# Performance work log

Measured on AMD Instinct MI355X. Metric: run time of the kernel, lower is better.

## Reference

```python
import jax, jax.numpy as jnp
import numpy as np
import math

N = 10000      # nodes (batched protein residues)
E = 160000     # edges (avg degree 16)
D = 1280       # node/hidden dim (ESM2-650M)
M = 24         # message_dim
EE = 16        # edge_embedding_dim (sinusoidal distance features)
L = 6          # num EGNN layers
LN_EPS = 1e-5


def setup_inputs() -> dict:
    key = jax.random.key(0)
    ks = jax.random.split(key, 20)
    s = 0.02
    h = jax.random.normal(ks[0], (N, D), jnp.float32)
    pos = jax.random.normal(ks[1], (N, 3), jnp.float32) * 10.0
    edge_index = jax.random.randint(ks[2], (2, E), 0, N, jnp.int32)
    msg_in_dim = 2 * D + EE + 1  # h_i, h_j, edge_attr, radial
    params = dict(
        node_emb_W=jax.random.normal(ks[3], (D, D), jnp.float32) * s,
        node_emb_b=jnp.zeros((D,), jnp.float32),
        msg_W1=jax.random.normal(ks[4], (L, msg_in_dim, M), jnp.float32) * s,
        msg_b1=jnp.zeros((L, M), jnp.float32),
        msg_W2=jax.random.normal(ks[5], (L, M, M), jnp.float32) * s,
        msg_b2=jnp.zeros((L, M), jnp.float32),
        coord_W1=jax.random.normal(ks[6], (L - 1, M, M), jnp.float32) * s,
        coord_b1=jnp.zeros((L - 1, M), jnp.float32),
        coord_W2=jax.random.normal(ks[7], (L - 1, M, 1), jnp.float32) * s,  # no bias
        node_W1=jax.random.normal(ks[8], (L, D + M, M), jnp.float32) * s,
        node_b1=jnp.zeros((L, M), jnp.float32),
        node_W2=jax.random.normal(ks[9], (L, M, D), jnp.float32) * s,
        node_b2=jnp.zeros((L, D), jnp.float32),
        ln_g=jnp.ones((L, D), jnp.float32),
        ln_b=jnp.zeros((L, D), jnp.float32),
    )
    return dict(h=h, pos=pos, edge_index=edge_index, **params)


def reference(h, pos, edge_index, node_emb_W, node_emb_b, msg_W1, msg_b1,
              msg_W2, msg_b2, coord_W1, coord_b1, coord_W2,
              node_W1, node_b1, node_W2, node_b2, ln_g, ln_b):
    row, col = edge_index[0], edge_index[1]  # PyG: row=source j, col=target i

    # sinusoidal distance embedding from initial coordinates (computed once)
    freqs = jnp.exp(-math.log(10000.0) * jnp.arange(0, EE, 2, dtype=jnp.float32) / EE)
    d0 = pos[row] - pos[col]                      # (E,3)
    dist = jnp.sqrt(jnp.sum(d0 * d0, axis=1))     # (E,)
    ang = dist[:, None] * freqs[None, :]          # (E, EE/2)
    edge_attr = jnp.stack([jnp.sin(ang), jnp.cos(ang)], axis=2).reshape(dist.shape[0], EE)

    h = h @ node_emb_W + node_emb_b

    # mean-aggregation denominator: in-degree of target nodes, clamped to 1
    deg = jax.ops.segment_sum(jnp.ones_like(dist), col, num_segments=N)
    denom = jnp.maximum(deg, 1.0)[:, None]

    for l in range(L):
        cd = pos[row] - pos[col]                  # (E,3) coord_diff
        radial = jnp.sum(cd * cd, axis=1, keepdims=True)
        msg_in = jnp.concatenate([h[col], h[row], edge_attr, radial], axis=-1)  # (E, 2D+EE+1)
        msg = jax.nn.silu(jax.nn.silu(msg_in @ msg_W1[l] + msg_b1[l]) @ msg_W2[l] + msg_b2[l])
        msg_agg = jax.ops.segment_sum(msg, col, num_segments=N) / denom  # scatter-mean
        if l < L - 1:  # update_coords for all but last layer
            w = jax.nn.silu(msg @ coord_W1[l] + coord_b1[l]) @ coord_W2[l]  # (E,1)
            pos = pos + jax.ops.segment_sum(cd * w, col, num_segments=N)   # index_add
        h_up = jax.nn.silu(jnp.concatenate([h, msg_agg], axis=-1) @ node_W1[l] + node_b1[l]) @ node_W2[l] + node_b2[l]
        hn = h + h_up
        mu = jnp.mean(hn, axis=-1, keepdims=True)
        var = jnp.mean((hn - mu) ** 2, axis=-1, keepdims=True)
        h = (hn - mu) / jnp.sqrt(var + LN_EPS) * ln_g[l] + ln_b[l]
        # dropout is identity in eval mode
    return h, pos
```

## Files before the change

### kernel.cpp

```cpp
#include <hip/hip_runtime.h>

#define NN 10000
#define NE 160000
#define DD 1280
#define MM 24

typedef __attribute__((ext_vector_type(8))) short bf16x8;
typedef __attribute__((ext_vector_type(4))) float f32x4;
typedef unsigned short u16;

#define O_nembW 0
#define O_nembB 1638400
#define O_msgW1 1639680
#define O_msgB1 2010880
#define O_msgW2 2011136
#define O_msgB2 2014592
#define O_cW1   2014848
#define O_cB1   2017792
#define O_cW2   2017920
#define O_nW1   2018048
#define O_nB1   2205824
#define O_nW2   2206080
#define O_nB2   2390400
#define O_lnG   2398080
#define O_lnB   2405760
#define TOTW    2413440

__device__ __forceinline__ float b2f(u16 u){
  union { unsigned int i; float f; } v; v.i = ((unsigned int)u) << 16; return v.f;
}
__device__ __forceinline__ u16 f2b(float f){
  union { float f; unsigned int i; } v; v.f = f;
  return (u16)((v.i + 0x7fffu + ((v.i >> 16) & 1u)) >> 16);
}
__device__ __forceinline__ float silu_f(float x){ return x / (1.f + __expf(-x)); }

__device__ __forceinline__ void gll16(const u16* g, u16* l){
  __builtin_amdgcn_global_load_lds(
      (const __attribute__((address_space(1))) void*)g,
      (__attribute__((address_space(3))) void*)l, 16, 0, 0);
}

__global__ __launch_bounds__(256) void k_sniff(const u16* __restrict__ h0, int* __restrict__ modep)
{
  __shared__ int cnt;
  if (threadIdx.x == 0) cnt = 0;
  __syncthreads();
  int local = 0;
  for (int i = threadIdx.x; i < 16384; i += 256){
    unsigned int e = (h0[i] >> 7) & 0xFF;
    if (e >= 0xE0) local++;
  }
  atomicAdd(&cnt, local);
  __syncthreads();
  if (threadIdx.x == 0) *modep = (cnt > 16) ? 0 : 1;
}

__global__ __launch_bounds__(256) void k_cvtw(const int* __restrict__ modep,
    const void* p0, const void* p1, const void* p2, const void* p3, const void* p4,
    const void* p5, const void* p6, const void* p7, const void* p8, const void* p9,
    const void* p10, const void* p11, const void* p12, const void* p13, const void* p14,
    u16* __restrict__ wbf)
{
  int i = blockIdx.x * 256 + threadIdx.x;
  if (i >= TOTW) return;
  int mode = *modep;
  const void* src; int j; int sz;
  if      (i < O_nembB){ src = p0;  j = i - O_nembW; sz = 1638400; }
  else if (i < O_msgW1){ src = p1;  j = i - O_nembB; sz = 1280; }
  else if (i < O_msgB1){ src = p2;  j = i - O_msgW1; sz = 371088; }
  else if (i < O_msgW2){ src = p3;  j = i - O_msgB1; sz = 144; }
  else if (i < O_msgB2){ src = p4;  j = i - O_msgW2; sz = 3456; }
  else if (i < O_cW1)  { src = p5;  j = i - O_msgB2; sz = 144; }
  else if (i < O_cB1)  { src = p6;  j = i - O_cW1;   sz = 2880; }
  else if (i < O_cW2)  { src = p7;  j = i - O_cB1;   sz = 120; }
  else if (i < O_nW1)  { src = p8;  j = i - O_cW2;   sz = 120; }
  else if (i < O_nB1)  { src = p9;  j = i - O_nW1;   sz = 187776; }
  else if (i < O_nW2)  { src = p10; j = i - O_nB1;   sz = 144; }
  else if (i < O_nB2)  { src = p11; j = i - O_nW2;   sz = 184320; }
  else if (i < O_lnG)  { src = p12; j = i - O_nB2;   sz = 7680; }
  else if (i < O_lnB)  { src = p13; j = i - O_lnG;   sz = 7680; }
  else                 { src = p14; j = i - O_lnB;   sz = 7680; }
  u16 v = 0;
  if (j < sz) v = mode ? ((const u16*)src)[j] : f2b(((const float*)src)[j]);
  wbf[i] = v;
}

__global__ __launch_bounds__(256) void k_tr(const u16* __restrict__ win, u16* __restrict__ wout)
{
  __shared__ u16 tile[32][33];
  int bx = blockIdx.x % 40, by = blockIdx.x / 40;
  int tc = threadIdx.x & 31, tr = threadIdx.x >> 5;
  #pragma unroll
  for (int p = 0; p < 4; p++){
    int r = p*8 + tr;
    tile[r][tc] = win[(size_t)(by*32 + r)*1280 + bx*32 + tc];
  }
  __syncthreads();
  #pragma unroll
  for (int p = 0; p < 4; p++){
    int r = p*8 + tr;
    wout[(size_t)(bx*32 + r)*1280 + by*32 + tc] = tile[tc][r];
  }
}

__global__ __launch_bounds__(256) void k_packproj(const u16* __restrict__ wbf, u16* __restrict__ wproj)
{
  int i = blockIdx.x * 256 + threadIdx.x;
  if (i >= 6*80*1280) return;
  int l = i / (80*1280);
  int rem = i - l*80*1280;
  int n = rem / 1280;
  int k = rem - n*1280;
  u16 v = 0;
  if (n < 24)       v = wbf[O_msgW1 + (size_t)l*2577*24 + (size_t)k*24 + n];
  else if (n < 48)  v = wbf[O_msgW1 + (size_t)l*2577*24 + (size_t)(1280+k)*24 + (n-24)];
  else if (n < 72)  v = wbf[O_nW1   + (size_t)l*1304*24 + (size_t)k*24 + (n-48)];
  wproj[i] = v;
}

__global__ __launch_bounds__(256) void k_packw2(const u16* __restrict__ wbf, u16* __restrict__ wn2p)
{
  int i = blockIdx.x * 256 + threadIdx.x;
  int l = i / (1280*32); int rem = i - l*1280*32;
  int n = rem >> 5, k = rem & 31;
  wn2p[i] = (k < 24) ? wbf[O_nW2 + (size_t)l*24*1280 + (size_t)k*1280 + n] : (u16)0;
}

__global__ __launch_bounds__(256) void k_cvth(const void* h0, const int* __restrict__ modep,
                                              u16* __restrict__ h0b)
{
  int i = blockIdx.x * 256 + threadIdx.x;
  if (*modep){
    ((int4*)h0b)[i] = ((const int4*)h0)[i];
  } else {
    const float* s = (const float*)h0 + (size_t)i*8;
    bf16x8 o;
    #pragma unroll
    for (int j = 0; j < 8; j++) o[j] = (short)f2b(s[j]);
    *(bf16x8*)(h0b + (size_t)i*8) = o;
  }
}

__global__ __launch_bounds__(256) void k_setup(const void* pos0, const int* __restrict__ modep,
    float* __restrict__ deg, float* __restrict__ posf, float* __restrict__ posf0)
{
  int i = blockIdx.x * 256 + threadIdx.x;
  int mode = *modep;
  if (i < NN) deg[i] = 0.f;
  if (i < NN * 3){
    float p = mode ? b2f(((const u16*)pos0)[i]) : ((const float*)pos0)[i];
    posf[i] = p; posf0[i] = p;
  }
}

__global__ __launch_bounds__(256) void k_deg(const int* __restrict__ eidx, float* __restrict__ deg)
{
  int e = blockIdx.x * 256 + threadIdx.x;
  atomicAdd(&deg[eidx[NE + e]], 1.f);
}

__global__ __launch_bounds__(256) void k_prefix(const float* __restrict__ deg,
                                                int* __restrict__ offs, int* __restrict__ cursor)
{
  __shared__ int part[256];
  int t = threadIdx.x;
  int lo = t * 40, hi = lo + 40; if (hi > NN) hi = NN; if (lo > NN) lo = NN;
  int s = 0;
  for (int i = lo; i < hi; i++) s += (int)deg[i];
  part[t] = s;
  __syncthreads();
  for (int off = 1; off < 256; off <<= 1){
    int v = (t >= off) ? part[t - off] : 0;
    __syncthreads();
    part[t] += v;
    __syncthreads();
  }
  int run = (t == 0) ? 0 : part[t - 1];
  for (int i = lo; i < hi; i++){
    offs[i] = run;
    run += (int)deg[i];
    cursor[i] = 0;
  }
  if (t == 255) offs[NN] = run;
}

__global__ __launch_bounds__(256) void k_scatter(const int* __restrict__ eidx,
    const int* __restrict__ offs, int* __restrict__ cursor, int* __restrict__ perm)
{
  int e = blockIdx.x * 256 + threadIdx.x;
  int cg = eidx[NE + e];
  int p = atomicAdd(&cursor[cg], 1);
  perm[offs[cg] + p] = e;
}

__global__ __launch_bounds__(256) void k_gemm_init(const u16* __restrict__ h0b,
    const u16* __restrict__ wembT, const u16* __restrict__ wbf, u16* __restrict__ Cb)
{
  __shared__ u16 As[128*32];
  __shared__ u16 Bs[128*32];
  int t = threadIdx.x;
  int lane = t & 63, wv = t >> 6;
  int bm = blockIdx.x % 79, bn = blockIdx.x / 79;
  int m0 = bm * 128, n0 = bn * 128;
  int col = lane & 15, quad = lane >> 4;
  int wm = wv & 1, wn = wv >> 1;
  f32x4 acc[4][4];
  #pragma unroll
  for (int mi = 0; mi < 4; mi++)
    #pragma unroll
    for (int ni = 0; ni < 4; ni++) acc[mi][ni] = (f32x4){0.f,0.f,0.f,0.f};

  for (int k0 = 0; k0 < DD; k0 += 32){
    #pragma unroll
    for (int is = 0; is < 2; is++){
      int flat = is*256 + t;
      int row = flat >> 2, seg = flat & 3;
      int grow = m0 + row; if (grow > NN-1) grow = NN-1;
      gll16(h0b + (size_t)grow*DD + k0 + seg*8, As + flat*8);
    }
    #pragma unroll
    for (int is = 0; is < 2; is++){
      int flat = is*256 + t;
      int row = flat >> 2, seg = flat & 3;
      gll16(wembT + (size_t)(n0 + row)*DD + k0 + seg*8, Bs + flat*8);
    }
    __builtin_amdgcn_s_waitcnt(0x0f70);
    __syncthreads();
    bf16x8 af[4], bfv[4];
    #pragma unroll
    for (int mi = 0; mi < 4; mi++)
      af[mi] = *(const bf16x8*)&As[(wm*64 + mi*16 + col)*32 + quad*8];
    #pragma unroll
    for (int ni = 0; ni < 4; ni++)
      bfv[ni] = *(const bf16x8*)&Bs[(wn*64 + ni*16 + col)*32 + quad*8];
    #pragma unroll
    for (int mi = 0; mi < 4; mi++)
      #pragma unroll
      for (int ni = 0; ni < 4; ni++)
        acc[mi][ni] = __builtin_amdgcn_mfma_f32_16x16x32_bf16(af[mi], bfv[ni], acc[mi][ni], 0, 0, 0);
    __syncthreads();
  }
  #pragma unroll
  for (int ni = 0; ni < 4; ni++){
    int cc = n0 + wn*64 + ni*16 + col;
    float bias = b2f(wbf[O_nembB + cc]);
    #pragma unroll
    for (int mi = 0; mi < 4; mi++){
      #pragma unroll
      for (int rr = 0; rr < 4; rr++){
        int row = m0 + wm*64 + mi*16 + quad*4 + rr;
        if (row < NN) Cb[(size_t)row*DD + cc] = f2b(acc[mi][ni][rr] + bias);
      }
    }
  }
}

__global__ __launch_bounds__(128) void k_gemm_proj(const u16* __restrict__ hbm,
    const u16* __restrict__ wproj, int layer,
    float* __restrict__ Ab, float* __restrict__ Bb, float* __restrict__ Mb)
{
  __shared__ u16 As[32*32];
  __shared__ u16 Bs[80*32];
  int t = threadIdx.x;
  int lane = t & 63, wv = t >> 6;
  int m0 = blockIdx.x * 32;
  int col = lane & 15, quad = lane >> 4;
  const u16* wp = wproj + (size_t)layer * 80 * 1280;
  f32x4 acc[5];
  #pragma unroll
  for (int ni = 0; ni < 5; ni++) acc[ni] = (f32x4){0.f,0.f,0.f,0.f};

  for (int k0 = 0; k0 < DD; k0 += 32){
    { int row = t >> 2, seg = t & 3;
      int grow = m0 + row; if (grow > NN-1) grow = NN-1;
      gll16(hbm + (size_t)grow*DD + k0 + seg*8, As + t*8); }
    #pragma unroll
    for (int is = 0; is < 3; is++){
      int flat = is*128 + t;
      if (flat < 320){
        int row = flat >> 2, seg = flat & 3;
        gll16(wp + (size_t)row*DD + k0 + seg*8, Bs + flat*8);
      }
    }
    __builtin_amdgcn_s_waitcnt(0x0f70);
    __syncthreads();
    bf16x8 af = *(const bf16x8*)&As[(wv*16 + col)*32 + quad*8];
    #pragma unroll
    for (int ni = 0; ni < 5; ni++){
      bf16x8 bv = *(const bf16x8*)&Bs[(ni*16 + col)*32 + quad*8];
      acc[ni] = __builtin_amdgcn_mfma_f32_16x16x32_bf16(af, bv, acc[ni], 0, 0, 0);
    }
    __syncthreads();
  }
  #pragma unroll
  for (int ni = 0; ni < 5; ni++){
    int n = ni*16 + col;
    if (n < 72){
      int rg = (n >= 48) ? 2 : (n >= 24 ? 1 : 0);
      int cc = n - rg*24;
      float* base = (rg == 0) ? Ab : (rg == 1) ? Bb : Mb;
      #pragma unroll
      for (int rr = 0; rr < 4; rr++){
        int m = m0 + wv*16 + quad*4 + rr;
        if (m < NN) base[m*24 + cc] = acc[ni][rr];
      }
    }
  }
}

__global__ __launch_bounds__(256) void k_edge(const int* __restrict__ eidx,
    const float* __restrict__ posf, const float* __restrict__ posf0,
    const float* __restrict__ Ab, const float* __restrict__ Bb,
    const u16* __restrict__ wbf, int layer, int do_coord,
    u16* __restrict__ msgu, float* __restrict__ wcdbuf)
{
  __shared__ float sW1e[16*24], sWr[24], sB1[24], sW2[24*24], sB2[24];
  __shared__ float sCW1[24*24], sCB1[24], sCW2[24];
  int t = threadIdx.x;
  const u16* w1l = wbf + O_msgW1 + (size_t)layer * 2577 * 24;
  for (int i = t; i < 16*24; i += 256) sW1e[i] = b2f(w1l[2560*24 + i]);
  for (int i = t; i < 24; i += 256){
    sWr[i] = b2f(w1l[2576*24 + i]);
    sB1[i] = b2f(wbf[O_msgB1 + layer*24 + i]);
    sB2[i] = b2f(wbf[O_msgB2 + layer*24 + i]);
  }
  for (int i = t; i < 576; i += 256) sW2[i] = b2f(wbf[O_msgW2 + layer*576 + i]);
  if (do_coord){
    for (int i = t; i < 576; i += 256) sCW1[i] = b2f(wbf[O_cW1 + layer*576 + i]);
    for (int i = t; i < 24; i += 256){
      sCB1[i] = b2f(wbf[O_cB1 + layer*24 + i]);
      sCW2[i] = b2f(wbf[O_cW2 + layer*24 + i]);
    }
  }
  __syncthreads();
  int e = blockIdx.x * 256 + t;
  int r = eidx[e], cg = eidx[NE + e];
  float cdx = posf[r*3+0] - posf[cg*3+0];
  float cdy = posf[r*3+1] - posf[cg*3+1];
  float cdz = posf[r*3+2] - posf[cg*3+2];
  float radial = cdx*cdx + cdy*cdy + cdz*cdz;
  float ex = posf0[r*3+0] - posf0[cg*3+0];
  float ey = posf0[r*3+1] - posf0[cg*3+1];
  float ez = posf0[r*3+2] - posf0[cg*3+2];
  float dist = sqrtf(ex*ex + ey*ey + ez*ez);
  const float FR[8] = {1.f, 0.31622776601683794f, 0.1f, 0.03162277660168379f,
                       0.01f, 0.0031622776601683794f, 0.001f, 0.00031622776601683794f};
  float eav[16];
  #pragma unroll
  for (int j = 0; j < 8; j++){
    float ang = dist * FR[j];
    eav[2*j]   = __sinf(ang);
    eav[2*j+1] = __cosf(ang);
  }
  float acc[24];
  const float4* ap  = (const float4*)(Ab + cg * 24);
  const float4* bp4 = (const float4*)(Bb + r * 24);
  #pragma unroll
  for (int q = 0; q < 6; q++){
    float4 a4 = ap[q], b4 = bp4[q];
    acc[q*4+0] = a4.x + b4.x; acc[q*4+1] = a4.y + b4.y;
    acc[q*4+2] = a4.z + b4.z; acc[q*4+3] = a4.w + b4.w;
  }
  #pragma unroll
  for (int m = 0; m < 24; m++) acc[m] += sB1[m] + radial * sWr[m];
  #pragma unroll
  for (int k = 0; k < 16; k++){
    #pragma unroll
    for (int m = 0; m < 24; m++) acc[m] += eav[k] * sW1e[k*24 + m];
  }
  #pragma unroll
  for (int m = 0; m < 24; m++) acc[m] = silu_f(acc[m]);
  float msg[24];
  #pragma unroll
  for (int m = 0; m < 24; m++){
    float v = sB2[m];
    #pragma unroll
    for (int k = 0; k < 24; k++) v += acc[k] * sW2[k*24 + m];
    msg[m] = silu_f(v);
  }
  {
    bf16x8 v0, v1, v2;
    #pragma unroll
    for (int j = 0; j < 8; j++){
      v0[j] = (short)f2b(msg[j]);
      v1[j] = (short)f2b(msg[8+j]);
      v2[j] = (short)f2b(msg[16+j]);
    }
    u16* mp = msgu + (size_t)e * 24;
    *(bf16x8*)(mp)      = v0;
    *(bf16x8*)(mp + 8)  = v1;
    *(bf16x8*)(mp + 16) = v2;
  }
  if (do_coord){
    float w = 0.f;
    #pragma unroll
    for (int m = 0; m < 24; m++){
      float v = sCB1[m];
      #pragma unroll
      for (int k = 0; k < 24; k++) v += msg[k] * sCW1[k*24 + m];
      w += silu_f(v) * sCW2[m];
    }
    wcdbuf[(size_t)e*3+0] = cdx * w;
    wcdbuf[(size_t)e*3+1] = cdy * w;
    wcdbuf[(size_t)e*3+2] = cdz * w;
  }
}

__global__ __launch_bounds__(256) void k_agg(const int* __restrict__ perm,
    const int* __restrict__ offs,
    const u16* __restrict__ msgu, const float* __restrict__ wcdbuf,
    float* __restrict__ magg, float* __restrict__ posf,
    int do_coord, int writeout, void* __restrict__ outp, const int* __restrict__ modep)
{
  int wv = threadIdx.x >> 6, lane = threadIdx.x & 63;
  int n = blockIdx.x * 4 + wv;
  int base = offs[n], cnt = offs[n+1] - base;
  float sum = 0.f;
  if (lane < 48){
    int m = (lane < 24) ? lane : lane - 24;
    for (int j = (lane < 24 ? 0 : 1); j < cnt; j += 2)
      sum += b2f(msgu[(size_t)perm[base+j]*24 + m]);
  }
  sum += __shfl_down(sum, 24, 64);
  if (lane < 24) magg[n*24 + lane] = sum;
  if (do_coord){
    float sc = 0.f;
    if (lane < 48){
      int c = lane % 3, jj = lane / 3;
      for (int j = jj; j < cnt; j += 16)
        sc += wcdbuf[(size_t)perm[base+j]*3 + c];
    }
    sc += __shfl_down(sc, 24, 64);
    sc += __shfl_down(sc, 12, 64);
    sc += __shfl_down(sc, 6, 64);
    sc += __shfl_down(sc, 3, 64);
    if (lane < 3){
      float p = posf[n*3 + lane] + sc;
      posf[n*3 + lane] = p;
      if (writeout){
        if (*modep) ((u16*)outp)[(size_t)NN*DD + n*3 + lane] = f2b(p);
        else        ((float*)outp)[(size_t)NN*DD + n*3 + lane] = p;
      }
    }
  }
}

__global__ __launch_bounds__(256) void k_combine(
    const float* __restrict__ Mb, const float* __restrict__ magg, const float* __restrict__ deg,
    const u16* __restrict__ wbf, const u16* __restrict__ wn2p, const int* __restrict__ modep,
    int layer, int last,
    u16* __restrict__ hbm, void* __restrict__ outp)
{
  __shared__ u16 shRes[16*1280];
  __shared__ u16 midb[16*32];
  __shared__ float sW1b[576], sB1c[24], sMg[384], sMbs[384], sDeg[16];
  __shared__ float wpart[4][16][2];
  __shared__ float mrow[16][2];
  int t = threadIdx.x;
  int lane = t & 63, wv = t >> 6;
  int row0 = blockIdx.x * 16;
  #pragma unroll
  for (int it = 0; it < 10; it++){
    int flat = it*256 + t;
    int r = flat / 160, off = (flat - r*160) * 8;
    gll16(hbm + (size_t)(row0 + r)*1280 + off, shRes + flat*8);
  }
  const u16* w1b = wbf + O_nW1 + (size_t)layer*1304*24 + 1280*24;
  for (int i = t; i < 576; i += 256) sW1b[i] = b2f(w1b[i]);
  if (t < 24) sB1c[t] = b2f(wbf[O_nB1 + layer*24 + t]);
  if (t < 16) sDeg[t] = 1.f / fmaxf(deg[row0 + t], 1.f);
  for (int i = t; i < 384; i += 256){ sMg[i] = magg[row0*24 + i]; sMbs[i] = Mb[row0*24 + i]; }
  midb[t] = 0; midb[256 + t] = 0;
  __builtin_amdgcn_s_waitcnt(0x0f70);
  __syncthreads();
  for (int o = t; o < 384; o += 256){
    int r = o / 24, m = o - r*24;
    float inv = sDeg[r];
    float a = sMbs[o] + sB1c[m];
    #pragma unroll
    for (int j = 0; j < 24; j++) a += sMg[r*24 + j] * inv * sW1b[j*24 + m];
    midb[r*32 + m] = f2b(silu_f(a));
  }
  __syncthreads();
  int col = lane & 15, quad = lane >> 4;
  bf16x8 af = *(const bf16x8*)&midb[col*32 + quad*8];
  int mode = *modep;
  float s1[4] = {0.f,0.f,0.f,0.f}, s2[4] = {0.f,0.f,0.f,0.f};
  float vals[20][4];
  const u16* wp = wn2p + (size_t)layer*1280*32;
  const u16* b2p = wbf + O_nB2 + (size_t)layer*1280;
  #pragma unroll
  for (int ti = 0; ti < 20; ti++){
    int n0 = wv*320 + ti*16;
    bf16x8 bfv = *(const bf16x8*)&wp[(size_t)(n0+col)*32 + quad*8];
    f32x4 acc = {0.f,0.f,0.f,0.f};
    acc = __builtin_amdgcn_mfma_f32_16x16x32_bf16(af, bfv, acc, 0, 0, 0);
    float b2 = b2f(b2p[n0 + col]);
    #pragma unroll
    for (int rr = 0; rr < 4; rr++){
      int r = quad*4 + rr;
      float hn = b2f(shRes[r*1280 + n0 + col]) + acc[rr] + b2;
      vals[ti][rr] = hn;
      s1[rr] += hn; s2[rr] += hn*hn;
    }
  }
  #pragma unroll
  for (int off = 1; off < 16; off <<= 1){
    #pragma unroll
    for (int rr = 0; rr < 4; rr++){
      s1[rr] += __shfl_xor(s1[rr], off, 64);
      s2[rr] += __shfl_xor(s2[rr], off, 64);
    }
  }
  if (col == 0){
    #pragma unroll
    for (int rr = 0; rr < 4; rr++){
      wpart[wv][quad*4+rr][0] = s1[rr];
      wpart[wv][quad*4+rr][1] = s2[rr];
    }
  }
  __syncthreads();
  if (t < 16){
    float S1 = wpart[0][t][0] + wpart[1][t][0] + wpart[2][t][0] + wpart[3][t][0];
    float S2 = wpart[0][t][1] + wpart[1][t][1] + wpart[2][t][1] + wpart[3][t][1];
    float mu = S1 * (1.f/1280.f);
    float var = S2 * (1.f/1280.f) - mu*mu;
    mrow[t][0] = mu;
    mrow[t][1] = rsqrtf(var + 1e-5f);
  }
  __syncthreads();
  const u16* gp = wbf + O_lnG + (size_t)layer*1280;
  const u16* bp = wbf + O_lnB + (size_t)layer*1280;
  #pragma unroll
  for (int ti = 0; ti < 20; ti++){
    int n0 = wv*320 + ti*16;
    int cc = n0 + col;
    float g  = b2f(gp[cc]);
    float bb = b2f(bp[cc]);
    #pragma unroll
    for (int rr = 0; rr < 4; rr++){
      int r = quad*4 + rr;
      float y = (vals[ti][rr] - mrow[r][0]) * mrow[r][1] * g + bb;
      hbm[(size_t)(row0 + r)*1280 + cc] = f2b(y);
      if (last){
        if (mode) ((u16*)outp)[(size_t)(row0+r)*1280 + cc] = f2b(y);
        else      ((float*)outp)[(size_t)(row0+r)*1280 + cc] = y;
      }
    }
  }
}

extern "C" void kernel_launch(void* const* d_in, const int* in_sizes, int n_in,
                              void* d_out, int out_size, void* d_ws, size_t ws_size,
                              hipStream_t stream)
{
  const void* h0    = d_in[0];
  const void* pos0  = d_in[1];
  const int*  eidx  = (const int*)d_in[2];

  char* w = (char*)d_ws;
  auto take = [&](size_t bytes)->char*{
    char* p = w; w += (bytes + 255) & ~(size_t)255; return p;
  };
  int*   modep  = (int*)  take(256);
  u16*   wbf    = (u16*)  take((size_t)TOTW * 2);
  u16*   wembT  = (u16*)  take((size_t)DD * DD * 2);
  u16*   wproj  = (u16*)  take((size_t)6 * 80 * 1280 * 2);
  u16*   wn2p   = (u16*)  take((size_t)6 * 1280 * 32 * 2);
  u16*   hbm    = (u16*)  take((size_t)NN * DD * 2);
  float* Ab     = (float*)take((size_t)NN * MM * 4);
  float* Bb     = (float*)take((size_t)NN * MM * 4);
  float* Mb     = (float*)take((size_t)NN * MM * 4);
  float* magg   = (float*)take((size_t)NN * MM * 4);
  float* deg    = (float*)take((size_t)NN * 4);
  float* posf   = (float*)take((size_t)NN * 3 * 4);
  float* posf0  = (float*)take((size_t)NN * 3 * 4);
  int*   offs   = (int*)  take((size_t)(NN + 1) * 4);
  int*   cursor = (int*)  take((size_t)NN * 4);
  int*   perm   = (int*)  take((size_t)NE * 4);

  u16*   h0b    = (u16*)d_out;
  u16*   msgu   = (u16*)d_out;
  float* wcdbuf = (float*)((char*)d_out + (size_t)NE * 24 * 2);

  k_sniff<<<1, 256, 0, stream>>>((const u16*)h0, modep);
  k_cvtw<<<(TOTW + 255)/256, 256, 0, stream>>>(modep,
      d_in[3], d_in[4], d_in[5], d_in[6], d_in[7], d_in[8], d_in[9], d_in[10],
      d_in[11], d_in[12], d_in[13], d_in[14], d_in[15], d_in[16], d_in[17], wbf);
  k_tr<<<1600, 256, 0, stream>>>(wbf + O_nembW, wembT);
  k_packproj<<<(6*80*1280 + 255)/256, 256, 0, stream>>>(wbf, wproj);
  k_packw2<<<6*1280*32/256, 256, 0, stream>>>(wbf, wn2p);
  k_cvth<<<NN*DD/8/256, 256, 0, stream>>>(h0, modep, h0b);
  k_setup<<<(NN*3 + 255)/256, 256, 0, stream>>>(pos0, modep, deg, posf, posf0);
  k_deg<<<NE/256, 256, 0, stream>>>(eidx, deg);
  k_prefix<<<1, 256, 0, stream>>>(deg, offs, cursor);
  k_scatter<<<NE/256, 256, 0, stream>>>(eidx, offs, cursor, perm);
  k_gemm_init<<<79*10, 256, 0, stream>>>(h0b, wembT, wbf, hbm);
  for (int l = 0; l < 6; l++){
    int dc = (l < 5) ? 1 : 0;
    k_gemm_proj<<<313, 128, 0, stream>>>(hbm, wproj, l, Ab, Bb, Mb);
    k_edge<<<NE/256, 256, 0, stream>>>(eidx, posf, posf0, Ab, Bb, wbf, l, dc, msgu, wcdbuf);
    k_agg<<<2500, 256, 0, stream>>>(perm, offs, msgu, wcdbuf, magg, posf,
                                    dc, (l == 4) ? 1 : 0, d_out, modep);
    k_combine<<<625, 256, 0, stream>>>(Mb, magg, deg, wbf, wn2p, modep, l, (l == 5) ? 1 : 0,
                                       hbm, d_out);
  }
}
```

Measured before the change: 858.5 us.

## Fuse next-layer projection into combine, write messages in CSR order, swizzle init GEMM

```diff
diff --git a/kernel.cpp b/kernel.cpp
--- a/kernel.cpp
+++ b/kernel.cpp
@@ -186,12 +186,12 @@
 }
 
 __global__ __launch_bounds__(256) void k_scatter(const int* __restrict__ eidx,
-    const int* __restrict__ offs, int* __restrict__ cursor, int* __restrict__ perm)
+    const int* __restrict__ offs, int* __restrict__ cursor, int* __restrict__ iperm)
 {
   int e = blockIdx.x * 256 + threadIdx.x;
   int cg = eidx[NE + e];
   int p = atomicAdd(&cursor[cg], 1);
-  perm[offs[cg] + p] = e;
+  iperm[e] = offs[cg] + p;
 }
 
 __global__ __launch_bounds__(256) void k_gemm_init(const u16* __restrict__ h0b,
@@ -199,9 +199,12 @@
 {
   __shared__ u16 As[128*32];
   __shared__ u16 Bs[128*32];
+  int bid = blockIdx.x;
+  int bm = (bid & 7) + 8 * (bid / 80);
+  int bn = (bid >> 3) % 10;
+  if (bm >= 79) return;
   int t = threadIdx.x;
   int lane = t & 63, wv = t >> 6;
-  int bm = blockIdx.x % 79, bn = blockIdx.x / 79;
   int m0 = bm * 128, n0 = bn * 128;
   int col = lane & 15, quad = lane >> 4;
   int wm = wv & 1, wn = wv >> 1;
@@ -310,6 +313,7 @@
 }
 
 __global__ __launch_bounds__(256) void k_edge(const int* __restrict__ eidx,
+    const int* __restrict__ iperm,
     const float* __restrict__ posf, const float* __restrict__ posf0,
     const float* __restrict__ Ab, const float* __restrict__ Bb,
     const u16* __restrict__ wbf, int layer, int do_coord,
@@ -336,6 +340,7 @@
   __syncthreads();
   int e = blockIdx.x * 256 + t;
   int r = eidx[e], cg = eidx[NE + e];
+  int slot = iperm[e];
   float cdx = posf[r*3+0] - posf[cg*3+0];
   float cdy = posf[r*3+1] - posf[cg*3+1];
   float cdz = posf[r*3+2] - posf[cg*3+2];
@@ -387,7 +392,7 @@
       v1[j] = (short)f2b(msg[8+j]);
       v2[j] = (short)f2b(msg[16+j]);
     }
-    u16* mp = msgu + (size_t)e * 24;
+    u16* mp = msgu + (size_t)slot * 24;
     *(bf16x8*)(mp)      = v0;
     *(bf16x8*)(mp + 8)  = v1;
     *(bf16x8*)(mp + 16) = v2;
@@ -401,14 +406,13 @@
       for (int k = 0; k < 24; k++) v += msg[k] * sCW1[k*24 + m];
       w += silu_f(v) * sCW2[m];
     }
-    wcdbuf[(size_t)e*3+0] = cdx * w;
-    wcdbuf[(size_t)e*3+1] = cdy * w;
-    wcdbuf[(size_t)e*3+2] = cdz * w;
-  }
-}
-
-__global__ __launch_bounds__(256) void k_agg(const int* __restrict__ perm,
-    const int* __restrict__ offs,
+    wcdbuf[(size_t)slot*3+0] = cdx * w;
+    wcdbuf[(size_t)slot*3+1] = cdy * w;
+    wcdbuf[(size_t)slot*3+2] = cdz * w;
+  }
+}
+
+__global__ __launch_bounds__(256) void k_agg(const int* __restrict__ offs,
     const u16* __restrict__ msgu, const float* __restrict__ wcdbuf,
     float* __restrict__ magg, float* __restrict__ posf,
     int do_coord, int writeout, void* __restrict__ outp, const int* __restrict__ modep)
@@ -420,7 +424,7 @@
   if (lane < 48){
     int m = (lane < 24) ? lane : lane - 24;
     for (int j = (lane < 24 ? 0 : 1); j < cnt; j += 2)
-      sum += b2f(msgu[(size_t)perm[base+j]*24 + m]);
+      sum += b2f(msgu[(size_t)(base+j)*24 + m]);
   }
   sum += __shfl_down(sum, 24, 64);
   if (lane < 24) magg[n*24 + lane] = sum;
@@ -429,7 +433,7 @@
     if (lane < 48){
       int c = lane % 3, jj = lane / 3;
       for (int j = jj; j < cnt; j += 16)
-        sc += wcdbuf[(size_t)perm[base+j]*3 + c];
+        sc += wcdbuf[(size_t)(base+j)*3 + c];
     }
     sc += __shfl_down(sc, 24, 64);
     sc += __shfl_down(sc, 12, 64);
@@ -447,12 +451,14 @@
 }
 
 __global__ __launch_bounds__(256) void k_combine(
-    const float* __restrict__ Mb, const float* __restrict__ magg, const float* __restrict__ deg,
-    const u16* __restrict__ wbf, const u16* __restrict__ wn2p, const int* __restrict__ modep,
-    int layer, int last,
-    u16* __restrict__ hbm, void* __restrict__ outp)
-{
-  __shared__ u16 shRes[16*1280];
+    float* __restrict__ Mb, const float* __restrict__ magg, const float* __restrict__ deg,
+    const u16* __restrict__ wbf, const u16* __restrict__ wn2p, const u16* __restrict__ wproj,
+    const int* __restrict__ modep,
+    int layer, int last, int fuse,
+    u16* __restrict__ hbm, void* __restrict__ outp,
+    float* __restrict__ Ab, float* __restrict__ Bb)
+{
+  __shared__ u16 ylds[16*1288];
   __shared__ u16 midb[16*32];
   __shared__ float sW1b[576], sB1c[24], sMg[384], sMbs[384], sDeg[16];
   __shared__ float wpart[4][16][2];
@@ -460,19 +466,12 @@
   int t = threadIdx.x;
   int lane = t & 63, wv = t >> 6;
   int row0 = blockIdx.x * 16;
-  #pragma unroll
-  for (int it = 0; it < 10; it++){
-    int flat = it*256 + t;
-    int r = flat / 160, off = (flat - r*160) * 8;
-    gll16(hbm + (size_t)(row0 + r)*1280 + off, shRes + flat*8);
-  }
   const u16* w1b = wbf + O_nW1 + (size_t)layer*1304*24 + 1280*24;
   for (int i = t; i < 576; i += 256) sW1b[i] = b2f(w1b[i]);
   if (t < 24) sB1c[t] = b2f(wbf[O_nB1 + layer*24 + t]);
   if (t < 16) sDeg[t] = 1.f / fmaxf(deg[row0 + t], 1.f);
   for (int i = t; i < 384; i += 256){ sMg[i] = magg[row0*24 + i]; sMbs[i] = Mb[row0*24 + i]; }
   midb[t] = 0; midb[256 + t] = 0;
-  __builtin_amdgcn_s_waitcnt(0x0f70);
   __syncthreads();
   for (int o = t; o < 384; o += 256){
     int r = o / 24, m = o - r*24;
@@ -488,19 +487,19 @@
   int mode = *modep;
   float s1[4] = {0.f,0.f,0.f,0.f}, s2[4] = {0.f,0.f,0.f,0.f};
   float vals[20][4];
-  const u16* wp = wn2p + (size_t)layer*1280*32;
+  const u16* wp2 = wn2p + (size_t)layer*1280*32;
   const u16* b2p = wbf + O_nB2 + (size_t)layer*1280;
   #pragma unroll
   for (int ti = 0; ti < 20; ti++){
     int n0 = wv*320 + ti*16;
-    bf16x8 bfv = *(const bf16x8*)&wp[(size_t)(n0+col)*32 + quad*8];
+    bf16x8 bfv = *(const bf16x8*)&wp2[(size_t)(n0+col)*32 + quad*8];
     f32x4 acc = {0.f,0.f,0.f,0.f};
     acc = __builtin_amdgcn_mfma_f32_16x16x32_bf16(af, bfv, acc, 0, 0, 0);
     float b2 = b2f(b2p[n0 + col]);
     #pragma unroll
     for (int rr = 0; rr < 4; rr++){
       int r = quad*4 + rr;
-      float hn = b2f(shRes[r*1280 + n0 + col]) + acc[rr] + b2;
+      float hn = b2f(hbm[(size_t)(row0 + r)*1280 + n0 + col]) + acc[rr] + b2;
       vals[ti][rr] = hn;
       s1[rr] += hn; s2[rr] += hn*hn;
     }
@@ -541,12 +540,42 @@
     #pragma unroll
     for (int rr = 0; rr < 4; rr++){
       int r = quad*4 + rr;
-      float y = (vals[ti][rr] - mrow[r][0]) * mrow[r][1] * g + bb;
-      hbm[(size_t)(row0 + r)*1280 + cc] = f2b(y);
+      u16 yb = f2b((vals[ti][rr] - mrow[r][0]) * mrow[r][1] * g + bb);
+      hbm[(size_t)(row0 + r)*1280 + cc] = yb;
+      if (fuse) ylds[r*1288 + cc] = yb;
       if (last){
-        if (mode) ((u16*)outp)[(size_t)(row0+r)*1280 + cc] = f2b(y);
-        else      ((float*)outp)[(size_t)(row0+r)*1280 + cc] = y;
+        if (mode) ((u16*)outp)[(size_t)(row0+r)*1280 + cc] = yb;
+        else      ((float*)outp)[(size_t)(row0+r)*1280 + cc] = b2f(yb);
       }
+    }
+  }
+  if (!fuse) return;
+  __syncthreads();
+  const u16* wp = wproj + (size_t)(layer+1) * 80 * 1280;
+  int nt1 = wv, nt2 = (wv == 0) ? 4 : -1;
+  f32x4 pa = {0.f,0.f,0.f,0.f}, pb = {0.f,0.f,0.f,0.f};
+  for (int k0 = 0; k0 < DD; k0 += 32){
+    bf16x8 af2 = *(const bf16x8*)&ylds[col*1288 + k0 + quad*8];
+    bf16x8 bv1 = *(const bf16x8*)&wp[(size_t)(nt1*16+col)*DD + k0 + quad*8];
+    pa = __builtin_amdgcn_mfma_f32_16x16x32_bf16(af2, bv1, pa, 0, 0, 0);
+    if (nt2 >= 0){
+      bf16x8 bv2 = *(const bf16x8*)&wp[(size_t)(nt2*16+col)*DD + k0 + quad*8];
+      pb = __builtin_amdgcn_mfma_f32_16x16x32_bf16(af2, bv2, pb, 0, 0, 0);
+    }
+  }
+  #pragma unroll
+  for (int pi = 0; pi < 2; pi++){
+    int tile = (pi == 0) ? nt1 : nt2;
+    if (tile < 0) continue;
+    f32x4 acc = (pi == 0) ? pa : pb;
+    int n = tile*16 + col;
+    if (n < 72){
+      int rg = (n >= 48) ? 2 : (n >= 24 ? 1 : 0);
+      int cc = n - rg*24;
+      float* base = (rg == 0) ? Ab : (rg == 1) ? Bb : Mb;
+      #pragma unroll
+      for (int rr = 0; rr < 4; rr++)
+        base[(row0 + quad*4 + rr)*24 + cc] = acc[rr];
     }
   }
 }
@@ -578,7 +607,7 @@
   float* posf0  = (float*)take((size_t)NN * 3 * 4);
   int*   offs   = (int*)  take((size_t)(NN + 1) * 4);
   int*   cursor = (int*)  take((size_t)NN * 4);
-  int*   perm   = (int*)  take((size_t)NE * 4);
+  int*   iperm  = (int*)  take((size_t)NE * 4);
 
   u16*   h0b    = (u16*)d_out;
   u16*   msgu   = (u16*)d_out;
@@ -595,15 +624,16 @@
   k_setup<<<(NN*3 + 255)/256, 256, 0, stream>>>(pos0, modep, deg, posf, posf0);
   k_deg<<<NE/256, 256, 0, stream>>>(eidx, deg);
   k_prefix<<<1, 256, 0, stream>>>(deg, offs, cursor);
-  k_scatter<<<NE/256, 256, 0, stream>>>(eidx, offs, cursor, perm);
-  k_gemm_init<<<79*10, 256, 0, stream>>>(h0b, wembT, wbf, hbm);
+  k_scatter<<<NE/256, 256, 0, stream>>>(eidx, offs, cursor, iperm);
+  k_gemm_init<<<800, 256, 0, stream>>>(h0b, wembT, wbf, hbm);
+  k_gemm_proj<<<313, 128, 0, stream>>>(hbm, wproj, 0, Ab, Bb, Mb);
   for (int l = 0; l < 6; l++){
     int dc = (l < 5) ? 1 : 0;
-    k_gemm_proj<<<313, 128, 0, stream>>>(hbm, wproj, l, Ab, Bb, Mb);
-    k_edge<<<NE/256, 256, 0, stream>>>(eidx, posf, posf0, Ab, Bb, wbf, l, dc, msgu, wcdbuf);
-    k_agg<<<2500, 256, 0, stream>>>(perm, offs, msgu, wcdbuf, magg, posf,
+    k_edge<<<NE/256, 256, 0, stream>>>(eidx, iperm, posf, posf0, Ab, Bb, wbf, l, dc, msgu, wcdbuf);
+    k_agg<<<2500, 256, 0, stream>>>(offs, msgu, wcdbuf, magg, posf,
                                     dc, (l == 4) ? 1 : 0, d_out, modep);
-    k_combine<<<625, 256, 0, stream>>>(Mb, magg, deg, wbf, wn2p, modep, l, (l == 5) ? 1 : 0,
-                                       hbm, d_out);
-  }
-}
+    k_combine<<<625, 256, 0, stream>>>(Mb, magg, deg, wbf, wn2p, wproj, modep,
+                                       l, (l == 5) ? 1 : 0, (l < 5) ? 1 : 0,
+                                       hbm, d_out, Ab, Bb);
+  }
+}
```

Result: slower. 880.8 us (+2.6%).
